# Kernel tuning notes

Measured on AMD Instinct MI355X. Metric: run time of the kernel, lower is better.

Reference implementation:

```python
import jax, jax.numpy as jnp
import numpy as np

GRAPH_DIM = 512
LLM_DIM = 4096
N_HEADS = 8
D_KEYS = 128
DK_H = N_HEADS * D_KEYS  # 1024


def setup_inputs() -> dict:
    key = jax.random.key(0)
    ks = jax.random.split(key, 12)
    B, L, S = 8, 1024, 1000
    sc = 0.02
    return {
        "target_embedding": jax.random.normal(ks[0], (B, L, GRAPH_DIM), jnp.float32),
        "source_embedding": jax.random.normal(ks[1], (S, LLM_DIM), jnp.float32),
        "value_embedding": jax.random.normal(ks[2], (S, LLM_DIM), jnp.float32),
        # weights stored as [in, out] (pre-transposed vs torch Linear)
        "Wq": jax.random.normal(ks[3], (GRAPH_DIM, DK_H), jnp.float32) * sc,
        "bq": jnp.zeros((DK_H,), jnp.float32),
        "Wk": jax.random.normal(ks[4], (LLM_DIM, DK_H), jnp.float32) * sc,
        "bk": jnp.zeros((DK_H,), jnp.float32),
        "Wv": jax.random.normal(ks[5], (LLM_DIM, DK_H), jnp.float32) * sc,
        "bv": jnp.zeros((DK_H,), jnp.float32),
        "Wo": jax.random.normal(ks[6], (DK_H, LLM_DIM), jnp.float32) * sc,
        "bo": jnp.zeros((LLM_DIM,), jnp.float32),
    }


def reference(target_embedding, source_embedding, value_embedding,
              Wq, bq, Wk, bk, Wv, bv, Wo, bo):
    B, L, _ = target_embedding.shape
    S, _ = source_embedding.shape
    H, E = N_HEADS, D_KEYS
    q = (target_embedding @ Wq + bq).reshape(B, L, H, E)   # blhe
    k = (source_embedding @ Wk + bk).reshape(S, H, E)      # she (batch-shared)
    v = (value_embedding @ Wv + bv).reshape(S, H, E)       # she (batch-shared)
    scale = 1.0 / jnp.sqrt(jnp.asarray(E, q.dtype))
    scores = jnp.einsum('blhe,she->bhls', q, k)            # [B,H,L,S]
    A = jax.nn.softmax(scale * scores, axis=-1)            # dropout = identity (eval)
    out = jnp.einsum('bhls,she->blhe', A, v).reshape(B, L, H * E)
    return out @ Wo + bo                                   # [B,L,llm_dim]
```

## Files before the change

### kernel.cpp

```cpp
#include <hip/hip_runtime.h>
#include <cstdint>
#include <cstddef>

typedef __bf16 bf16;
typedef __bf16 bf16x4 __attribute__((ext_vector_type(4)));
typedef __bf16 bf16x8 __attribute__((ext_vector_type(8)));
typedef float f32x4 __attribute__((ext_vector_type(4)));


__device__ __forceinline__ void gload_lds16(const void* g, void* l) {
    typedef __attribute__((address_space(1))) void gv;
    typedef __attribute__((address_space(3))) void lv;
    __builtin_amdgcn_global_load_lds((gv*)g, (lv*)l, 16, 0, 0);
}

__global__ __launch_bounds__(256) void cast3_f32_bf16(
    const float* __restrict__ in0, bf16* __restrict__ out0,
    const float* __restrict__ in1, bf16* __restrict__ out1,
    const float* __restrict__ in2, bf16* __restrict__ out2)
{
    const int which = blockIdx.y;
    const float* in = which == 0 ? in0 : which == 1 ? in1 : in2;
    bf16* out       = which == 0 ? out0 : which == 1 ? out1 : out2;
    const size_t n_in = which == 0 ? (size_t)8192 * 512 : (size_t)1000 * 4096;

    const size_t i = ((size_t)blockIdx.x * 256 + threadIdx.x) * 8;
    f32x4 a = (f32x4){0.f, 0.f, 0.f, 0.f};
    f32x4 b = (f32x4){0.f, 0.f, 0.f, 0.f};
    if (i < n_in) {
        a = *(const f32x4*)(in + i);
        b = *(const f32x4*)(in + i + 4);
    }
    bf16x8 o;
    o[0] = (bf16)a[0]; o[1] = (bf16)a[1]; o[2] = (bf16)a[2]; o[3] = (bf16)a[3];
    o[4] = (bf16)b[0]; o[5] = (bf16)b[1]; o[6] = (bf16)b[2]; o[7] = (bf16)b[3];
    *(bf16x8*)(out + i) = o;
}

__global__ __launch_bounds__(256) void transpose4(
    const float* __restrict__ Wq, bf16* __restrict__ WqT,
    const float* __restrict__ Wk, bf16* __restrict__ WkT,
    const float* __restrict__ Wv, bf16* __restrict__ WvT,
    const float* __restrict__ Wo, bf16* __restrict__ WoT)
{
    int id = blockIdx.x;
    const float* in; bf16* out; int R, C, bx, by;
    if (id < 512)       { in = Wq; out = WqT; R = 512;  C = 1024; bx = id % 32;  by = id / 32; }
    else if (id < 4608) { id -= 512;  in = Wk; out = WkT; R = 4096; C = 1024; bx = id % 32;  by = id / 32; }
    else if (id < 8704) { id -= 4608; in = Wv; out = WvT; R = 4096; C = 1024; bx = id % 32;  by = id / 32; }
    else                { id -= 8704; in = Wo; out = WoT; R = 1024; C = 4096; bx = id % 128; by = id / 128; }

    __shared__ bf16 tile[32][33];
    const int tx = threadIdx.x & 31, ty = threadIdx.x >> 5;
    const int c0 = bx * 32, r0 = by * 32;
    #pragma unroll
    for (int i = ty; i < 32; i += 8)
        tile[i][tx] = (bf16)in[(size_t)(r0 + i) * C + (c0 + tx)];
    __syncthreads();
    #pragma unroll
    for (int i = ty; i < 32; i += 8)
        out[(size_t)(c0 + i) * R + (r0 + tx)] = tile[tx][i];
}

__global__ __launch_bounds__(256, 3) void gemm_bt(
    const bf16* __restrict__ A, const bf16* __restrict__ Bt,
    const float* __restrict__ bias, void* __restrict__ Cv,
    int M, int N, int K, int lda, int ldb, int ldc, int outF32)
{
    __shared__ __align__(16) bf16 As[128 * 64];
    __shared__ __align__(16) bf16 Bs[128 * 64];

    const int tid = threadIdx.x;
    const int w = tid >> 6, ln = tid & 63;

    const int gx = gridDim.x, gy = gridDim.y;
    int bm, bn;
    if (((gx & 7) | (gy & 7)) == 0) {
        const int orig = blockIdx.y * gx + blockIdx.x;
        const int xcd = orig & 7, t = orig >> 3;
        const int nsb_x = gx >> 3;
        const int s = xcd + 8 * (t >> 6);
        const int win = t & 63;
        bm = (s / nsb_x) * 8 + (win >> 3);
        bn = (s % nsb_x) * 8 + (win & 7);
    } else {
        bm = blockIdx.y; bn = blockIdx.x;
    }

    const int wm = (w >> 1) * 64, wn = (w & 1) * 64;
    const int rgrp = ln >> 4, cl = ln & 15;

    f32x4 acc[4][4];
    #pragma unroll
    for (int mt = 0; mt < 4; ++mt)
        #pragma unroll
        for (int nt = 0; nt < 4; ++nt)
            acc[mt][nt] = (f32x4){0.f, 0.f, 0.f, 0.f};

    for (int k0 = 0; k0 < K; k0 += 64) {
        #pragma unroll
        for (int j = 0; j < 4; ++j) {
            const int t2 = tid + 256 * j;
            const int row = t2 >> 3;
            const int ch = (t2 & 7) ^ (row & 7);
            int arow = bm * 128 + row;
            if (arow > M - 1) arow = M - 1;
            gload_lds16(A + (size_t)arow * lda + k0 + ch * 8,
                        (char*)As + j * 4096 + w * 1024);
            const int brow = bn * 128 + row;
            gload_lds16(Bt + (size_t)brow * ldb + k0 + ch * 8,
                        (char*)Bs + j * 4096 + w * 1024);
        }
        __syncthreads();

        #pragma unroll
        for (int kk = 0; kk < 2; ++kk) {
            bf16x8 af[4], bfr[4];
            #pragma unroll
            for (int mt = 0; mt < 4; ++mt) {
                const int row = wm + mt * 16 + cl;
                const int ch = (kk * 4 + rgrp) ^ (row & 7);
                af[mt] = *(const bf16x8*)(As + row * 64 + ch * 8);
            }
            #pragma unroll
            for (int nt = 0; nt < 4; ++nt) {
                const int row = wn + nt * 16 + cl;
                const int ch = (kk * 4 + rgrp) ^ (row & 7);
                bfr[nt] = *(const bf16x8*)(Bs + row * 64 + ch * 8);
            }
            #pragma unroll
            for (int mt = 0; mt < 4; ++mt)
                #pragma unroll
                for (int nt = 0; nt < 4; ++nt)
                    acc[mt][nt] = __builtin_amdgcn_mfma_f32_16x16x32_bf16(
                        bfr[nt], af[mt], acc[mt][nt], 0, 0, 0);
        }
        __syncthreads();
    }

    #pragma unroll
    for (int nt = 0; nt < 4; ++nt) {
        const int col0 = bn * 128 + wn + nt * 16 + rgrp * 4;
        const f32x4 bv4 = bias ? *(const f32x4*)(bias + col0)
                               : (f32x4){0.f, 0.f, 0.f, 0.f};
        #pragma unroll
        for (int mt = 0; mt < 4; ++mt) {
            const int row = bm * 128 + wm + mt * 16 + cl;
            if (row < M) {
                const f32x4 v = acc[mt][nt] + bv4;
                if (outF32) {
                    __builtin_nontemporal_store(
                        v, (f32x4*)((float*)Cv + (size_t)row * ldc + col0));
                } else {
                    bf16x4 h;
                    h[0] = (bf16)v[0]; h[1] = (bf16)v[1];
                    h[2] = (bf16)v[2]; h[3] = (bf16)v[3];
                    *(bf16x4*)((bf16*)Cv + (size_t)row * ldc + col0) = h;
                }
            }
        }
    }
}

__global__ __launch_bounds__(256, 4) void gemm_kv(
    const bf16* __restrict__ A0, const bf16* __restrict__ Bt0,
    const float* __restrict__ b0, bf16* __restrict__ C0,
    const bf16* __restrict__ A1, const bf16* __restrict__ Bt1,
    const float* __restrict__ b1, bf16* __restrict__ C1)
{
    const int sel = blockIdx.z;
    const bf16* A  = sel ? A1 : A0;
    const bf16* Bt = sel ? Bt1 : Bt0;
    const float* bias = sel ? b1 : b0;
    bf16* Cv = sel ? C1 : C0;
    const int transC = sel;
    const int K = 4096, lda = 4096, ldb = 4096, ldc = 1024;

    __shared__ __align__(16) bf16 As[64 * 64];
    __shared__ __align__(16) bf16 Bs[64 * 64];

    const int tid = threadIdx.x;
    const int w = tid >> 6, ln = tid & 63;
    const int bm = blockIdx.y, bn = blockIdx.x;
    const int wm = (w >> 1) * 32, wn = (w & 1) * 32;
    const int rgrp = ln >> 4, cl = ln & 15;

    f32x4 acc[2][2];
    #pragma unroll
    for (int mt = 0; mt < 2; ++mt)
        #pragma unroll
        for (int nt = 0; nt < 2; ++nt)
            acc[mt][nt] = (f32x4){0.f, 0.f, 0.f, 0.f};

    for (int k0 = 0; k0 < K; k0 += 64) {
        #pragma unroll
        for (int j = 0; j < 2; ++j) {
            const int arow = bm * 64 + j * 32 + w * 8 + (ln >> 3);
            const bf16* ag = A + (size_t)arow * lda + k0 + (ln & 7) * 8;
            gload_lds16(ag, (char*)As + j * 4096 + w * 1024);
            const int brow = bn * 64 + j * 32 + w * 8 + (ln >> 3);
            const bf16* bg = Bt + (size_t)brow * ldb + k0 + (ln & 7) * 8;
            gload_lds16(bg, (char*)Bs + j * 4096 + w * 1024);
        }
        __syncthreads();

        bf16x8 af[2][2], bfr[2][2];
        #pragma unroll
        for (int mt = 0; mt < 2; ++mt)
            #pragma unroll
            for (int kk = 0; kk < 2; ++kk)
                af[mt][kk] = *(const bf16x8*)(As + (wm + mt * 16 + cl) * 64 + kk * 32 + rgrp * 8);
        #pragma unroll
        for (int nt = 0; nt < 2; ++nt)
            #pragma unroll
            for (int kk = 0; kk < 2; ++kk)
                bfr[nt][kk] = *(const bf16x8*)(Bs + (wn + nt * 16 + cl) * 64 + kk * 32 + rgrp * 8);
        #pragma unroll
        for (int mt = 0; mt < 2; ++mt)
            #pragma unroll
            for (int nt = 0; nt < 2; ++nt)
                #pragma unroll
                for (int kk = 0; kk < 2; ++kk)
                    acc[mt][nt] = __builtin_amdgcn_mfma_f32_16x16x32_bf16(
                        af[mt][kk], bfr[nt][kk], acc[mt][nt], 0, 0, 0);
        __syncthreads();
    }

    #pragma unroll
    for (int nt = 0; nt < 2; ++nt) {
        const int col = bn * 64 + wn + nt * 16 + cl;
        const float bvv = bias[col];
        #pragma unroll
        for (int mt = 0; mt < 2; ++mt) {
            #pragma unroll
            for (int reg = 0; reg < 4; ++reg) {
                const int row = bm * 64 + wm + mt * 16 + rgrp * 4 + reg;
                const float v = acc[mt][nt][reg] + bvv;
                const size_t idx = transC ? (size_t)col * ldc + row
                                          : (size_t)row * ldc + col;
                Cv[idx] = (bf16)v;
            }
        }
    }
}

__global__ __launch_bounds__(256) void flash_attn(
    const bf16* __restrict__ Q, const bf16* __restrict__ Kb,
    const bf16* __restrict__ Vt, bf16* __restrict__ O)
{
    const int tid = threadIdx.x;
    const int w = tid >> 6, ln = tid & 63;
    const int b = blockIdx.x >> 3, h = blockIdx.x & 7;
    const int l0 = blockIdx.y * 128 + w * 32;
    const int rgrp = ln >> 4, cl = ln & 15;
    const float sl2 = 0.08838834764831845f * 1.44269504088896340736f;

    __shared__ __align__(16) bf16 Ks[2][32 * 128];
    __shared__ __align__(16) bf16 Vs[2][128 * 32];
    __shared__ __align__(16) bf16 Pl[4][2][16 * 40];

    bf16x8 qf[2][4];
    #pragma unroll
    for (int m = 0; m < 2; ++m) {
        const bf16* qp = Q + (size_t)(b * 1024 + l0 + m * 16 + cl) * 1024 + h * 128 + rgrp * 8;
        #pragma unroll
        for (int kk = 0; kk < 4; ++kk) qf[m][kk] = *(const bf16x8*)(qp + kk * 32);
    }

    f32x4 o[2][8];
    #pragma unroll
    for (int m = 0; m < 2; ++m)
        #pragma unroll
        for (int nt = 0; nt < 8; ++nt) o[m][nt] = (f32x4){0.f, 0.f, 0.f, 0.f};
    float m_[2] = {-1e30f, -1e30f};
    float l_[2] = {0.f, 0.f};

    auto stage = [&](int bi, int t) {
        const int s0 = t * 32;
        #pragma unroll
        for (int c = 0; c < 2; ++c) {
            {
                const int r = c * 16 + w * 4 + (ln >> 4);
                const int e = ((ln & 15) ^ (r & 7)) << 3;
                gload_lds16(Kb + (size_t)(s0 + r) * 1024 + h * 128 + e,
                            (char*)Ks[bi] + c * 4096 + w * 1024);
            }
            {
                const int r = c * 64 + w * 16 + (ln >> 2);
                const int sc = ((ln & 3) ^ (r & 3)) << 3;
                gload_lds16(Vt + (size_t)(h * 128 + r) * 1024 + s0 + sc,
                            (char*)Vs[bi] + c * 4096 + w * 1024);
            }
        }
    };

    stage(0, 0);

    for (int t = 0; t < 32; ++t) {
        __syncthreads();
        if (t < 31) stage((t + 1) & 1, t + 1);
        const int bi = t & 1;
        const int s0 = t * 32;
        const bf16* Kt = Ks[bi];
        const bf16* Vtl = Vs[bi];

        bf16x8 kf[2][4];
        #pragma unroll
        for (int half = 0; half < 2; ++half) {
            const int row = half * 16 + cl;
            #pragma unroll
            for (int kk = 0; kk < 4; ++kk) {
                const int pos = (kk * 4 + rgrp) ^ (row & 7);
                kf[half][kk] = *(const bf16x8*)((const char*)Kt + row * 256 + pos * 16);
            }
        }

        f32x4 st[2][2];
        __builtin_amdgcn_s_setprio(1);
        #pragma unroll
        for (int m = 0; m < 2; ++m)
            #pragma unroll
            for (int half = 0; half < 2; ++half) {
                f32x4 sc = (f32x4){0.f, 0.f, 0.f, 0.f};
                #pragma unroll
                for (int kk = 0; kk < 4; ++kk)
                    sc = __builtin_amdgcn_mfma_f32_16x16x32_bf16(
                        kf[half][kk], qf[m][kk], sc, 0, 0, 0);
                st[m][half] = sc;
            }
        __builtin_amdgcn_s_setprio(0);

        #pragma unroll
        for (int m = 0; m < 2; ++m) {
            float z[8];
            #pragma unroll
            for (int half = 0; half < 2; ++half)
                #pragma unroll
                for (int reg = 0; reg < 4; ++reg) {
                    const int sg = s0 + half * 16 + rgrp * 4 + reg;
                    z[half * 4 + reg] = (sg < 1000) ? st[m][half][reg] * sl2 : -1e30f;
                }
            float mx = fmaxf(fmaxf(fmaxf(z[0], z[1]), fmaxf(z[2], z[3])),
                             fmaxf(fmaxf(z[4], z[5]), fmaxf(z[6], z[7])));
            mx = fmaxf(mx, __shfl_xor(mx, 16));
            mx = fmaxf(mx, __shfl_xor(mx, 32));
            if (__any(mx > m_[m] + 8.0f)) {
                const float mnew = fmaxf(m_[m], mx);
                const float alpha = __builtin_amdgcn_exp2f(m_[m] - mnew);
                m_[m] = mnew;
                l_[m] *= alpha;
                #pragma unroll
                for (int reg = 0; reg < 4; ++reg) {
                    const float ar = __shfl(alpha, rgrp * 4 + reg);
                    #pragma unroll
                    for (int nt = 0; nt < 8; ++nt) o[m][nt][reg] *= ar;
                }
            }
            float p[8];
            float rs = 0.f;
            #pragma unroll
            for (int i = 0; i < 8; ++i) {
                p[i] = __builtin_amdgcn_exp2f(z[i] - m_[m]);
                rs += p[i];
            }
            rs += __shfl_xor(rs, 16);
            rs += __shfl_xor(rs, 32);
            l_[m] += rs;
            #pragma unroll
            for (int half = 0; half < 2; ++half) {
                bf16x4 pk;
                #pragma unroll
                for (int reg = 0; reg < 4; ++reg) pk[reg] = (bf16)p[half * 4 + reg];
                *(bf16x4*)(&Pl[w][m][cl * 40 + half * 16 + rgrp * 4]) = pk;
            }
        }

        bf16x8 vf[8];
        #pragma unroll
        for (int nt = 0; nt < 8; ++nt) {
            const int row = nt * 16 + cl;
            const int pos = rgrp ^ (row & 3);
            vf[nt] = *(const bf16x8*)((const char*)Vtl + row * 64 + pos * 16);
        }

        __builtin_amdgcn_s_setprio(1);
        #pragma unroll
        for (int m = 0; m < 2; ++m) {
            const bf16x8 pa = *(const bf16x8*)(&Pl[w][m][cl * 40 + rgrp * 8]);
            #pragma unroll
            for (int nt = 0; nt < 8; ++nt)
                o[m][nt] = __builtin_amdgcn_mfma_f32_16x16x32_bf16(
                    pa, vf[nt], o[m][nt], 0, 0, 0);
        }
        __builtin_amdgcn_s_setprio(0);
    }

    #pragma unroll
    for (int m = 0; m < 2; ++m) {
        #pragma unroll
        for (int reg = 0; reg < 4; ++reg) {
            const float inv = __builtin_amdgcn_rcpf(__shfl(l_[m], rgrp * 4 + reg));
            const int row = l0 + m * 16 + rgrp * 4 + reg;
            #pragma unroll
            for (int nt = 0; nt < 8; ++nt) {
                const int col = h * 128 + nt * 16 + cl;
                O[(size_t)(b * 1024 + row) * 1024 + col] = (bf16)(o[m][nt][reg] * inv);
            }
        }
    }
}

extern "C" void kernel_launch(void* const* d_in, const int* in_sizes, int n_in,
                              void* d_out, int out_size, void* d_ws, size_t ws_size,
                              hipStream_t stream)
{
    const float* target = (const float*)d_in[0];
    const float* source = (const float*)d_in[1];
    const float* value  = (const float*)d_in[2];
    const float* Wq = (const float*)d_in[3];
    const float* bq = (const float*)d_in[4];
    const float* Wk = (const float*)d_in[5];
    const float* bk = (const float*)d_in[6];
    const float* Wv = (const float*)d_in[7];
    const float* bv = (const float*)d_in[8];
    const float* Wo = (const float*)d_in[9];
    const float* bo = (const float*)d_in[10];

    char* po = (char*)d_out;
    size_t off = 0;
    bf16* tgt_b = (bf16*)(po + off); off += (size_t)8192 * 512 * 2;
    bf16* src_b = (bf16*)(po + off); off += (size_t)1024 * 4096 * 2;
    bf16* val_b = (bf16*)(po + off); off += (size_t)1024 * 4096 * 2;
    bf16* WqT   = (bf16*)(po + off); off += (size_t)1024 * 512 * 2;
    bf16* WkT   = (bf16*)(po + off); off += (size_t)1024 * 4096 * 2;
    bf16* WvT   = (bf16*)(po + off); off += (size_t)1024 * 4096 * 2;
    bf16* Qb    = (bf16*)(po + off); off += (size_t)8192 * 1024 * 2;
    bf16* Kb    = (bf16*)(po + off); off += (size_t)1024 * 1024 * 2;
    bf16* Vt    = (bf16*)(po + off); off += (size_t)1024 * 1024 * 2;
    char* ws = (char*)d_ws;
    bf16* AO  = (bf16*)ws;
    bf16* WoT = (bf16*)(ws + (size_t)8192 * 1024 * 2);

    cast3_f32_bf16<<<dim3(2048, 3), 256, 0, stream>>>(
        target, tgt_b, source, src_b, value, val_b);

    transpose4<<<12800, 256, 0, stream>>>(Wq, WqT, Wk, WkT, Wv, WvT, Wo, WoT);

    gemm_bt<<<dim3(8, 64), 256, 0, stream>>>(tgt_b, WqT, bq, Qb, 8192, 1024, 512, 512, 512, 1024, 0);
    gemm_kv<<<dim3(16, 16, 2), 256, 0, stream>>>(
        src_b, WkT, bk, Kb, val_b, WvT, bv, Vt);

    flash_attn<<<dim3(64, 8), 256, 0, stream>>>(Qb, Kb, Vt, AO);

    gemm_bt<<<dim3(32, 64), 256, 0, stream>>>(AO, WoT, bo, d_out, 8192, 4096, 1024, 1024, 1024, 4096, 1);

    (void)in_sizes; (void)n_in; (void)out_size; (void)ws_size;
}
```

Before: 454.3 us.

## Swizzle GEMM LDS tiles and double the attention KV tile per barrier

The GEMM kernel now XOR-swizzles the 16-byte chunks of its A and B tiles in shared memory, both when loading from global memory and when reading fragments, to reduce LDS bank conflicts. The flash attention kernel stages two 32-row K/V tiles per double-buffer slot and processes both between barriers, halving the number of __syncthreads. It also removes the s_setprio hints. The trade-off is twice the K/V LDS footprint (about 64KB plus the P buffers), which can lower occupancy.

```diff
diff --git a/kernel.cpp b/kernel.cpp
--- a/kernel.cpp
+++ b/kernel.cpp
@@ -195,12 +195,15 @@
     for (int k0 = 0; k0 < K; k0 += 64) {
         #pragma unroll
         for (int j = 0; j < 2; ++j) {
-            const int arow = bm * 64 + j * 32 + w * 8 + (ln >> 3);
-            const bf16* ag = A + (size_t)arow * lda + k0 + (ln & 7) * 8;
-            gload_lds16(ag, (char*)As + j * 4096 + w * 1024);
-            const int brow = bn * 64 + j * 32 + w * 8 + (ln >> 3);
-            const bf16* bg = Bt + (size_t)brow * ldb + k0 + (ln & 7) * 8;
-            gload_lds16(bg, (char*)Bs + j * 4096 + w * 1024);
+            const int t2 = tid + 256 * j;
+            const int row = t2 >> 3;
+            const int ch = (t2 & 7) ^ (row & 7);
+            const int arow = bm * 64 + row;
+            gload_lds16(A + (size_t)arow * lda + k0 + ch * 8,
+                        (char*)As + j * 4096 + w * 1024);
+            const int brow = bn * 64 + row;
+            gload_lds16(Bt + (size_t)brow * ldb + k0 + ch * 8,
+                        (char*)Bs + j * 4096 + w * 1024);
         }
         __syncthreads();
 
@@ -208,13 +211,19 @@
         #pragma unroll
         for (int mt = 0; mt < 2; ++mt)
             #pragma unroll
-            for (int kk = 0; kk < 2; ++kk)
-                af[mt][kk] = *(const bf16x8*)(As + (wm + mt * 16 + cl) * 64 + kk * 32 + rgrp * 8);
+            for (int kk = 0; kk < 2; ++kk) {
+                const int row = wm + mt * 16 + cl;
+                const int ch = (kk * 4 + rgrp) ^ (row & 7);
+                af[mt][kk] = *(const bf16x8*)(As + row * 64 + ch * 8);
+            }
         #pragma unroll
         for (int nt = 0; nt < 2; ++nt)
             #pragma unroll
-            for (int kk = 0; kk < 2; ++kk)
-                bfr[nt][kk] = *(const bf16x8*)(Bs + (wn + nt * 16 + cl) * 64 + kk * 32 + rgrp * 8);
+            for (int kk = 0; kk < 2; ++kk) {
+                const int row = wn + nt * 16 + cl;
+                const int ch = (kk * 4 + rgrp) ^ (row & 7);
+                bfr[nt][kk] = *(const bf16x8*)(Bs + row * 64 + ch * 8);
+            }
         #pragma unroll
         for (int mt = 0; mt < 2; ++mt)
             #pragma unroll
@@ -255,8 +264,8 @@
     const int rgrp = ln >> 4, cl = ln & 15;
     const float sl2 = 0.08838834764831845f * 1.44269504088896340736f;
 
-    __shared__ __align__(16) bf16 Ks[2][32 * 128];
-    __shared__ __align__(16) bf16 Vs[2][128 * 32];
+    __shared__ __align__(16) bf16 Ks[2][2][32 * 128];
+    __shared__ __align__(16) bf16 Vs[2][2][128 * 32];
     __shared__ __align__(16) bf16 Pl[4][2][16 * 40];
 
     bf16x8 qf[2][4];
@@ -275,7 +284,7 @@
     float m_[2] = {-1e30f, -1e30f};
     float l_[2] = {0.f, 0.f};
 
-    auto stage = [&](int bi, int t) {
+    auto stage = [&](int bi, int slot, int t) {
         const int s0 = t * 32;
         #pragma unroll
         for (int c = 0; c < 2; ++c) {
@@ -283,116 +292,121 @@
                 const int r = c * 16 + w * 4 + (ln >> 4);
                 const int e = ((ln & 15) ^ (r & 7)) << 3;
                 gload_lds16(Kb + (size_t)(s0 + r) * 1024 + h * 128 + e,
-                            (char*)Ks[bi] + c * 4096 + w * 1024);
+                            (char*)Ks[bi][slot] + c * 4096 + w * 1024);
             }
             {
                 const int r = c * 64 + w * 16 + (ln >> 2);
                 const int sc = ((ln & 3) ^ (r & 3)) << 3;
                 gload_lds16(Vt + (size_t)(h * 128 + r) * 1024 + s0 + sc,
-                            (char*)Vs[bi] + c * 4096 + w * 1024);
+                            (char*)Vs[bi][slot] + c * 4096 + w * 1024);
             }
         }
     };
 
-    stage(0, 0);
-
-    for (int t = 0; t < 32; ++t) {
+    stage(0, 0, 0);
+    stage(0, 1, 1);
+    int buf = 0;
+
+    for (int tp = 0; tp < 16; ++tp) {
         __syncthreads();
-        if (t < 31) stage((t + 1) & 1, t + 1);
-        const int bi = t & 1;
-        const int s0 = t * 32;
-        const bf16* Kt = Ks[bi];
-        const bf16* Vtl = Vs[bi];
-
-        bf16x8 kf[2][4];
-        #pragma unroll
-        for (int half = 0; half < 2; ++half) {
-            const int row = half * 16 + cl;
-            #pragma unroll
-            for (int kk = 0; kk < 4; ++kk) {
-                const int pos = (kk * 4 + rgrp) ^ (row & 7);
-                kf[half][kk] = *(const bf16x8*)((const char*)Kt + row * 256 + pos * 16);
-            }
-        }
-
-        f32x4 st[2][2];
-        __builtin_amdgcn_s_setprio(1);
-        #pragma unroll
-        for (int m = 0; m < 2; ++m)
+        if (tp < 15) {
+            stage(buf ^ 1, 0, 2 * tp + 2);
+            stage(buf ^ 1, 1, 2 * tp + 3);
+        }
+
+        #pragma unroll
+        for (int u = 0; u < 2; ++u) {
+            const int s0 = (2 * tp + u) * 32;
+            const bf16* Kt = Ks[buf][u];
+            const bf16* Vtl = Vs[buf][u];
+
+            bf16x8 kf[2][4];
             #pragma unroll
             for (int half = 0; half < 2; ++half) {
-                f32x4 sc = (f32x4){0.f, 0.f, 0.f, 0.f};
-                #pragma unroll
-                for (int kk = 0; kk < 4; ++kk)
-                    sc = __builtin_amdgcn_mfma_f32_16x16x32_bf16(
-                        kf[half][kk], qf[m][kk], sc, 0, 0, 0);
-                st[m][half] = sc;
-            }
-        __builtin_amdgcn_s_setprio(0);
-
-        #pragma unroll
-        for (int m = 0; m < 2; ++m) {
-            float z[8];
-            #pragma unroll
-            for (int half = 0; half < 2; ++half)
-                #pragma unroll
-                for (int reg = 0; reg < 4; ++reg) {
-                    const int sg = s0 + half * 16 + rgrp * 4 + reg;
-                    z[half * 4 + reg] = (sg < 1000) ? st[m][half][reg] * sl2 : -1e30f;
-                }
-            float mx = fmaxf(fmaxf(fmaxf(z[0], z[1]), fmaxf(z[2], z[3])),
-                             fmaxf(fmaxf(z[4], z[5]), fmaxf(z[6], z[7])));
-            mx = fmaxf(mx, __shfl_xor(mx, 16));
-            mx = fmaxf(mx, __shfl_xor(mx, 32));
-            if (__any(mx > m_[m] + 8.0f)) {
-                const float mnew = fmaxf(m_[m], mx);
-                const float alpha = __builtin_amdgcn_exp2f(m_[m] - mnew);
-                m_[m] = mnew;
-                l_[m] *= alpha;
-                #pragma unroll
-                for (int reg = 0; reg < 4; ++reg) {
-                    const float ar = __shfl(alpha, rgrp * 4 + reg);
+                const int row = half * 16 + cl;
+                #pragma unroll
+                for (int kk = 0; kk < 4; ++kk) {
+                    const int pos = (kk * 4 + rgrp) ^ (row & 7);
+                    kf[half][kk] = *(const bf16x8*)((const char*)Kt + row * 256 + pos * 16);
+                }
+            }
+
+            f32x4 st[2][2];
+            #pragma unroll
+            for (int m = 0; m < 2; ++m)
+                #pragma unroll
+                for (int half = 0; half < 2; ++half) {
+                    f32x4 sc = (f32x4){0.f, 0.f, 0.f, 0.f};
                     #pragma unroll
-                    for (int nt = 0; nt < 8; ++nt) o[m][nt][reg] *= ar;
-                }
-            }
-            float p[8];
-            float rs = 0.f;
-            #pragma unroll
-            for (int i = 0; i < 8; ++i) {
-                p[i] = __builtin_amdgcn_exp2f(z[i] - m_[m]);
-                rs += p[i];
-            }
-            rs += __shfl_xor(rs, 16);
-            rs += __shfl_xor(rs, 32);
-            l_[m] += rs;
-            #pragma unroll
-            for (int half = 0; half < 2; ++half) {
-                bf16x4 pk;
-                #pragma unroll
-                for (int reg = 0; reg < 4; ++reg) pk[reg] = (bf16)p[half * 4 + reg];
-                *(bf16x4*)(&Pl[w][m][cl * 40 + half * 16 + rgrp * 4]) = pk;
-            }
-        }
-
-        bf16x8 vf[8];
-        #pragma unroll
-        for (int nt = 0; nt < 8; ++nt) {
-            const int row = nt * 16 + cl;
-            const int pos = rgrp ^ (row & 3);
-            vf[nt] = *(const bf16x8*)((const char*)Vtl + row * 64 + pos * 16);
-        }
-
-        __builtin_amdgcn_s_setprio(1);
-        #pragma unroll
-        for (int m = 0; m < 2; ++m) {
-            const bf16x8 pa = *(const bf16x8*)(&Pl[w][m][cl * 40 + rgrp * 8]);
-            #pragma unroll
-            for (int nt = 0; nt < 8; ++nt)
-                o[m][nt] = __builtin_amdgcn_mfma_f32_16x16x32_bf16(
-                    pa, vf[nt], o[m][nt], 0, 0, 0);
-        }
-        __builtin_amdgcn_s_setprio(0);
+                    for (int kk = 0; kk < 4; ++kk)
+                        sc = __builtin_amdgcn_mfma_f32_16x16x32_bf16(
+                            kf[half][kk], qf[m][kk], sc, 0, 0, 0);
+                    st[m][half] = sc;
+                }
+
+            #pragma unroll
+            for (int m = 0; m < 2; ++m) {
+                float z[8];
+                #pragma unroll
+                for (int half = 0; half < 2; ++half)
+                    #pragma unroll
+                    for (int reg = 0; reg < 4; ++reg) {
+                        const int sg = s0 + half * 16 + rgrp * 4 + reg;
+                        z[half * 4 + reg] = (sg < 1000) ? st[m][half][reg] * sl2 : -1e30f;
+                    }
+                float mx = fmaxf(fmaxf(fmaxf(z[0], z[1]), fmaxf(z[2], z[3])),
+                                 fmaxf(fmaxf(z[4], z[5]), fmaxf(z[6], z[7])));
+                mx = fmaxf(mx, __shfl_xor(mx, 16));
+                mx = fmaxf(mx, __shfl_xor(mx, 32));
+                if (__any(mx > m_[m] + 8.0f)) {
+                    const float mnew = fmaxf(m_[m], mx);
+                    const float alpha = __builtin_amdgcn_exp2f(m_[m] - mnew);
+                    m_[m] = mnew;
+                    l_[m] *= alpha;
+                    #pragma unroll
+                    for (int reg = 0; reg < 4; ++reg) {
+                        const float ar = __shfl(alpha, rgrp * 4 + reg);
+                        #pragma unroll
+                        for (int nt = 0; nt < 8; ++nt) o[m][nt][reg] *= ar;
+                    }
+                }
+                float p[8];
+                float rs = 0.f;
+                #pragma unroll
+                for (int i = 0; i < 8; ++i) {
+                    p[i] = __builtin_amdgcn_exp2f(z[i] - m_[m]);
+                    rs += p[i];
+                }
+                rs += __shfl_xor(rs, 16);
+                rs += __shfl_xor(rs, 32);
+                l_[m] += rs;
+                #pragma unroll
+                for (int half = 0; half < 2; ++half) {
+                    bf16x4 pk;
+                    #pragma unroll
+                    for (int reg = 0; reg < 4; ++reg) pk[reg] = (bf16)p[half * 4 + reg];
+                    *(bf16x4*)(&Pl[w][m][cl * 40 + half * 16 + rgrp * 4]) = pk;
+                }
+            }
+
+            bf16x8 vf[8];
+            #pragma unroll
+            for (int nt = 0; nt < 8; ++nt) {
+                const int row = nt * 16 + cl;
+                const int pos = rgrp ^ (row & 3);
+                vf[nt] = *(const bf16x8*)((const char*)Vtl + row * 64 + pos * 16);
+            }
+
+            #pragma unroll
+            for (int m = 0; m < 2; ++m) {
+                const bf16x8 pa = *(const bf16x8*)(&Pl[w][m][cl * 40 + rgrp * 8]);
+                #pragma unroll
+                for (int nt = 0; nt < 8; ++nt)
+                    o[m][nt] = __builtin_amdgcn_mfma_f32_16x16x32_bf16(
+                        pa, vf[nt], o[m][nt], 0, 0, 0);
+            }
+        }
+        buf ^= 1;
     }
 
     #pragma unroll
```

Result: faster. 404.9 us (-10.9%).
